# Kernel tuning notes

Measured on AMD Instinct MI355X. Metric: run time of the kernel, lower is better.

The kernel has to match this reference:

```python
import jax, jax.numpy as jnp
import numpy as np

B, S, H = 32, 512, 1024
N_CAND = 256
NUM_LABELS = 34


def setup_inputs() -> dict:
    key = jax.random.key(0)
    k1, k2, k3, k4 = jax.random.split(key, 4)
    hidden = jax.random.normal(k1, (B, S, H), dtype=jnp.float32)
    W = jax.random.normal(k2, (2 * H, NUM_LABELS), dtype=jnp.float32) * 0.02
    b = jnp.zeros((NUM_LABELS,), dtype=jnp.float32)
    cand_batch = jax.random.randint(k3, (N_CAND,), 0, B, dtype=jnp.int32)
    # cut positions in [1, S-1] so both left and right segments are non-empty
    cand_cut = jax.random.randint(k4, (N_CAND,), 1, S, dtype=jnp.int32)
    return {"hidden": hidden, "W": W, "b": b,
            "cand_batch": cand_batch, "cand_cut": cand_cut}


def reference(hidden, W, b, cand_batch, cand_cut):
    # hidden: [B, S, H]; cand_batch/cand_cut: [N]
    S_ = hidden.shape[1]
    x = hidden[cand_batch]                      # [N, S, H] per-candidate sequence
    pos = jnp.arange(S_)                        # [S]
    left = (pos[None, :, None] < cand_cut[:, None, None])  # [N, S, 1]
    neg = jnp.finfo(hidden.dtype).min
    pooledL = jnp.max(jnp.where(left, x, neg), axis=1)      # [N, H] max over tokens < cut
    pooledR = jnp.max(jnp.where(left, neg, x), axis=1)      # [N, H] max over tokens >= cut
    pooled = jnp.concatenate([pooledL, pooledR], axis=-1)   # [N, 2H]
    logits = pooled @ W + b                                  # [N, num_labels]
    return logits
```

## Files before the change

### kernel.cpp

```cpp
#include <hip/hip_runtime.h>
#include <cfloat>


constexpr int S_LEN  = 512;
constexpr int HDIM   = 1024;
constexpr int NLAB   = 34;
constexpr int CHUNK  = 16;
constexpr int NCHUNK = S_LEN / CHUNK;
constexpr int PSDIM  = NCHUNK + 1;

__device__ __forceinline__ void fmax4(float4& a, const float4 v) {
    a.x = fmaxf(a.x, v.x); a.y = fmaxf(a.y, v.y);
    a.z = fmaxf(a.z, v.z); a.w = fmaxf(a.w, v.w);
}

__global__ __launch_bounds__(256) void chunkmax_kernel(
    const float* __restrict__ hidden, float* __restrict__ cm)
{
    const int blk = blockIdx.x;
    const int b   = blk / NCHUNK;
    const int c   = blk % NCHUNK;
    const int t   = threadIdx.x;

    const float* base = hidden + ((size_t)b * S_LEN + (size_t)c * CHUNK) * HDIM + 4 * t;
    float4 m = make_float4(-FLT_MAX, -FLT_MAX, -FLT_MAX, -FLT_MAX);
    #pragma unroll
    for (int s = 0; s < CHUNK; ++s)
        fmax4(m, *reinterpret_cast<const float4*>(base + (size_t)s * HDIM));

    *reinterpret_cast<float4*>(cm + ((size_t)b * NCHUNK + c) * HDIM + 4 * t) = m;
}

__global__ __launch_bounds__(128) void prefsuf_kernel(
    const float* __restrict__ cm,
    float* __restrict__ pref,
    float* __restrict__ suff)
{
    const int b    = blockIdx.x;
    const int q    = blockIdx.y;
    const int tx   = threadIdx.x;
    const int dir  = tx >> 6;
    const int lane = tx & 63;
    const int col  = q * 256 + 4 * lane;

    const float* cmb = cm + (size_t)b * NCHUNK * HDIM + col;
    float4 run = make_float4(-FLT_MAX, -FLT_MAX, -FLT_MAX, -FLT_MAX);

    if (dir == 0) {
        float* pb = pref + (size_t)b * PSDIM * HDIM + col;
        *reinterpret_cast<float4*>(pb) = run;
        #pragma unroll 8
        for (int c = 0; c < NCHUNK; ++c) {
            fmax4(run, *reinterpret_cast<const float4*>(cmb + (size_t)c * HDIM));
            *reinterpret_cast<float4*>(pb + (size_t)(c + 1) * HDIM) = run;
        }
    } else {
        float* sb = suff + (size_t)b * PSDIM * HDIM + col;
        *reinterpret_cast<float4*>(sb + (size_t)NCHUNK * HDIM) = run;
        #pragma unroll 8
        for (int c = NCHUNK - 1; c >= 0; --c) {
            fmax4(run, *reinterpret_cast<const float4*>(cmb + (size_t)c * HDIM));
            *reinterpret_cast<float4*>(sb + (size_t)c * HDIM) = run;
        }
    }
}

__global__ __launch_bounds__(1024) void pool_gemm3(
    const float* __restrict__ hidden,
    const float* __restrict__ pref,
    const float* __restrict__ suff,
    const float* __restrict__ W,
    const float* __restrict__ bias,
    const int*   __restrict__ cand_batch,
    const int*   __restrict__ cand_cut,
    float*       __restrict__ out)
{
    __shared__ float partL[4][HDIM];
    __shared__ float partR[4][HDIM];
    __shared__ float pooled[2 * HDIM];
    __shared__ float gpart[16][NLAB];

    const int n   = blockIdx.x;
    const int t   = threadIdx.x;
    const int g   = t >> 8;
    const int tt  = t & 255;
    const int col = 4 * tt;
    const int b   = cand_batch[n];
    const int cut = cand_cut[n];
    const int fcL = cut >> 4;
    const int rem = cut & 15;
    const int fcR = fcL + (rem ? 1 : 0);

    float4 mL = make_float4(-FLT_MAX, -FLT_MAX, -FLT_MAX, -FLT_MAX);
    float4 mR = mL;

    if (g == 0)
        mL = *reinterpret_cast<const float4*>(
            pref + ((size_t)b * PSDIM + fcL) * HDIM + col);
    else if (g == 1)
        mR = *reinterpret_cast<const float4*>(
            suff + ((size_t)b * PSDIM + fcR) * HDIM + col);

    if (rem) {
        const int base16 = fcL * CHUNK;
        const float* hbase = hidden + (size_t)b * S_LEN * HDIM + col;
        #pragma unroll
        for (int i = 0; i < 4; ++i) {
            const int s = base16 + g + 4 * i;
            const float4 v = *reinterpret_cast<const float4*>(hbase + (size_t)s * HDIM);
            if (s < cut) fmax4(mL, v); else fmax4(mR, v);
        }
    }

    *reinterpret_cast<float4*>(&partL[g][col]) = mL;
    *reinterpret_cast<float4*>(&partR[g][col]) = mR;
    __syncthreads();

    pooled[t] = fmaxf(fmaxf(partL[0][t], partL[1][t]),
                      fmaxf(partL[2][t], partL[3][t]));
    pooled[HDIM + t] = fmaxf(fmaxf(partR[0][t], partR[1][t]),
                             fmaxf(partR[2][t], partR[3][t]));
    __syncthreads();

    const int w    = t >> 6;
    const int lane = t & 63;
    if (lane < NLAB) {
        const float* p  = pooled + 128 * w;
        const float* Wp = W + (size_t)(128 * w) * NLAB + lane;
        float acc = 0.0f;
        #pragma unroll 8
        for (int k = 0; k < 128; ++k)
            acc = fmaf(p[k], Wp[(size_t)k * NLAB], acc);
        gpart[w][lane] = acc;
    }
    __syncthreads();

    if (t < NLAB) {
        float s = bias[t];
        #pragma unroll
        for (int w2 = 0; w2 < 16; ++w2) s += gpart[w2][t];
        out[(size_t)n * NLAB + t] = s;
    }
}

__global__ __launch_bounds__(256) void dmbert_pool_gemm(
    const float* __restrict__ hidden,
    const float* __restrict__ W,
    const float* __restrict__ bias,
    const int*   __restrict__ cand_batch,
    const int*   __restrict__ cand_cut,
    float*       __restrict__ out)
{
    __shared__ float pooled[2 * HDIM];
    __shared__ float partial[4][NLAB];

    const int n   = blockIdx.x;
    const int t   = threadIdx.x;
    const int bi  = cand_batch[n];
    const int cut = cand_cut[n];

    const float* base = hidden + (size_t)bi * S_LEN * HDIM + 4 * t;
    float4 mL = make_float4(-FLT_MAX, -FLT_MAX, -FLT_MAX, -FLT_MAX);
    float4 mR = mL;

    #pragma unroll 4
    for (int s = 0; s < cut; ++s)
        fmax4(mL, *reinterpret_cast<const float4*>(base + (size_t)s * HDIM));
    #pragma unroll 4
    for (int s = cut; s < S_LEN; ++s)
        fmax4(mR, *reinterpret_cast<const float4*>(base + (size_t)s * HDIM));

    *reinterpret_cast<float4*>(&pooled[4 * t])        = mL;
    *reinterpret_cast<float4*>(&pooled[HDIM + 4 * t]) = mR;
    __syncthreads();

    const int w    = t >> 6;
    const int lane = t & 63;
    if (lane < NLAB) {
        const int k0 = w * (2 * HDIM / 4);
        float acc = 0.0f;
        #pragma unroll 8
        for (int k = k0; k < k0 + (2 * HDIM / 4); ++k)
            acc = fmaf(pooled[k], W[(size_t)k * NLAB + lane], acc);
        partial[w][lane] = acc;
    }
    __syncthreads();

    if (t < NLAB) {
        out[(size_t)n * NLAB + t] =
            partial[0][t] + partial[1][t] + partial[2][t] + partial[3][t] + bias[t];
    }
}

extern "C" void kernel_launch(void* const* d_in, const int* in_sizes, int n_in,
                              void* d_out, int out_size, void* d_ws, size_t ws_size,
                              hipStream_t stream) {
    const float* hidden = (const float*)d_in[0];
    const float* W      = (const float*)d_in[1];
    const float* bias   = (const float*)d_in[2];
    const int*   cb     = (const int*)d_in[3];
    const int*   cc     = (const int*)d_in[4];
    float*       outp   = (float*)d_out;

    const int ncand = in_sizes[3];
    const int B     = in_sizes[0] / (S_LEN * HDIM);
    const size_t cm_elems = (size_t)B * NCHUNK * HDIM;
    const size_t ps_elems = (size_t)B * PSDIM * HDIM;
    const size_t ws_needed = (cm_elems + 2 * ps_elems) * sizeof(float);

    if (ws_size >= ws_needed) {
        float* cm   = (float*)d_ws;
        float* pref = cm + cm_elems;
        float* suff = pref + ps_elems;
        chunkmax_kernel<<<B * NCHUNK, 256, 0, stream>>>(hidden, cm);
        prefsuf_kernel<<<dim3(B, 4), 128, 0, stream>>>(cm, pref, suff);
        pool_gemm3<<<ncand, 1024, 0, stream>>>(hidden, pref, suff, W, bias, cb, cc, outp);
    } else {
        dmbert_pool_gemm<<<ncand, 256, 0, stream>>>(hidden, W, bias, cb, cc, outp);
    }
}
```

Baseline: 110.0 us.

## Fuse chunk-max and prefix/suffix scan into one kernel with shared-memory scan

Merges the chunk-max kernel and the serial prefix/suffix kernel into one kernel. Each block handles one batch row and a 128-column slice, computes all 32 chunk maxima, then runs a log-step Hillis-Steele scan in shared memory for both directions. This removes the intermediate chunk-max buffer round trip, one kernel launch, and the poorly parallel serial scan, which ran on only 128 blocks of 128 threads. In exchange the grid is 256 blocks of 1024 threads with several barriers per scan step.

Measured after the change: 110.0 us. About the same (-0.0%).

```diff
diff --git a/kernel.cpp b/kernel.cpp
--- a/kernel.cpp
+++ b/kernel.cpp
@@ -8,61 +8,60 @@
 constexpr int CHUNK  = 16;
 constexpr int NCHUNK = S_LEN / CHUNK;
 constexpr int PSDIM  = NCHUNK + 1;
+constexpr int SLICE  = 128;
 
 __device__ __forceinline__ void fmax4(float4& a, const float4 v) {
     a.x = fmaxf(a.x, v.x); a.y = fmaxf(a.y, v.y);
     a.z = fmaxf(a.z, v.z); a.w = fmaxf(a.w, v.w);
 }
 
-__global__ __launch_bounds__(256) void chunkmax_kernel(
-    const float* __restrict__ hidden, float* __restrict__ cm)
+__global__ __launch_bounds__(1024) void prefsuf_fused(
+    const float* __restrict__ hidden,
+    float* __restrict__ pref,
+    float* __restrict__ suff)
 {
-    const int blk = blockIdx.x;
-    const int b   = blk / NCHUNK;
-    const int c   = blk % NCHUNK;
-    const int t   = threadIdx.x;
-
-    const float* base = hidden + ((size_t)b * S_LEN + (size_t)c * CHUNK) * HDIM + 4 * t;
+    __shared__ float4 pm[NCHUNK][32];
+    __shared__ float4 sm[NCHUNK][32];
+
+    const int b     = blockIdx.x;
+    const int slice = blockIdx.y;
+    const int t     = threadIdx.x;
+    const int c     = t >> 5;
+    const int j     = t & 31;
+    const int col   = slice * SLICE + 4 * j;
+
+    const float* base = hidden + ((size_t)b * S_LEN + (size_t)c * CHUNK) * HDIM + col;
     float4 m = make_float4(-FLT_MAX, -FLT_MAX, -FLT_MAX, -FLT_MAX);
     #pragma unroll
     for (int s = 0; s < CHUNK; ++s)
         fmax4(m, *reinterpret_cast<const float4*>(base + (size_t)s * HDIM));
 
-    *reinterpret_cast<float4*>(cm + ((size_t)b * NCHUNK + c) * HDIM + 4 * t) = m;
-}
-
-__global__ __launch_bounds__(128) void prefsuf_kernel(
-    const float* __restrict__ cm,
-    float* __restrict__ pref,
-    float* __restrict__ suff)
-{
-    const int b    = blockIdx.x;
-    const int q    = blockIdx.y;
-    const int tx   = threadIdx.x;
-    const int dir  = tx >> 6;
-    const int lane = tx & 63;
-    const int col  = q * 256 + 4 * lane;
-
-    const float* cmb = cm + (size_t)b * NCHUNK * HDIM + col;
-    float4 run = make_float4(-FLT_MAX, -FLT_MAX, -FLT_MAX, -FLT_MAX);
-
-    if (dir == 0) {
-        float* pb = pref + (size_t)b * PSDIM * HDIM + col;
-        *reinterpret_cast<float4*>(pb) = run;
-        #pragma unroll 8
-        for (int c = 0; c < NCHUNK; ++c) {
-            fmax4(run, *reinterpret_cast<const float4*>(cmb + (size_t)c * HDIM));
-            *reinterpret_cast<float4*>(pb + (size_t)(c + 1) * HDIM) = run;
-        }
-    } else {
-        float* sb = suff + (size_t)b * PSDIM * HDIM + col;
-        *reinterpret_cast<float4*>(sb + (size_t)NCHUNK * HDIM) = run;
-        #pragma unroll 8
-        for (int c = NCHUNK - 1; c >= 0; --c) {
-            fmax4(run, *reinterpret_cast<const float4*>(cmb + (size_t)c * HDIM));
-            *reinterpret_cast<float4*>(sb + (size_t)c * HDIM) = run;
-        }
-    }
+    pm[c][j] = m;
+    sm[c][j] = m;
+    __syncthreads();
+
+    #pragma unroll
+    for (int d = 1; d < NCHUNK; d <<= 1) {
+        float4 a = pm[c][j];
+        if (c >= d)          fmax4(a, pm[c - d][j]);
+        float4 s = sm[c][j];
+        if (c + d < NCHUNK)  fmax4(s, sm[c + d][j]);
+        __syncthreads();
+        pm[c][j] = a;
+        sm[c][j] = s;
+        __syncthreads();
+    }
+
+    const float4 ninf = make_float4(-FLT_MAX, -FLT_MAX, -FLT_MAX, -FLT_MAX);
+    float* pb = pref + ((size_t)b * PSDIM) * HDIM + col;
+    float* sb = suff + ((size_t)b * PSDIM) * HDIM + col;
+
+    *reinterpret_cast<float4*>(pb + (size_t)(c + 1) * HDIM) = pm[c][j];
+    *reinterpret_cast<float4*>(sb + (size_t)c * HDIM)       = sm[c][j];
+    if (c == 0)
+        *reinterpret_cast<float4*>(pb) = ninf;
+    if (c == NCHUNK - 1)
+        *reinterpret_cast<float4*>(sb + (size_t)NCHUNK * HDIM) = ninf;
 }
 
 __global__ __launch_bounds__(1024) void pool_gemm3(
@@ -204,16 +203,13 @@
 
     const int ncand = in_sizes[3];
     const int B     = in_sizes[0] / (S_LEN * HDIM);
-    const size_t cm_elems = (size_t)B * NCHUNK * HDIM;
-    const size_t ps_elems = (size_t)B * PSDIM * HDIM;
-    const size_t ws_needed = (cm_elems + 2 * ps_elems) * sizeof(float);
+    const size_t ps_elems  = (size_t)B * PSDIM * HDIM;
+    const size_t ws_needed = 2 * ps_elems * sizeof(float);
 
     if (ws_size >= ws_needed) {
-        float* cm   = (float*)d_ws;
-        float* pref = cm + cm_elems;
+        float* pref = (float*)d_ws;
         float* suff = pref + ps_elems;
-        chunkmax_kernel<<<B * NCHUNK, 256, 0, stream>>>(hidden, cm);
-        prefsuf_kernel<<<dim3(B, 4), 128, 0, stream>>>(cm, pref, suff);
+        prefsuf_fused<<<dim3(B, HDIM / SLICE), 1024, 0, stream>>>(hidden, pref, suff);
         pool_gemm3<<<ncand, 1024, 0, stream>>>(hidden, pref, suff, W, bias, cb, cc, outp);
     } else {
         dmbert_pool_gemm<<<ncand, 256, 0, stream>>>(hidden, W, bias, cb, cc, outp);
```
